# Performance work log

Hardware: AMD Instinct MI355X
Metric: run time of the kernel (lower is better)

The kernel has to match this reference:

```python
import jax, jax.numpy as jnp
import numpy as np

TOP_K = 5


def setup_inputs() -> dict:
    key = jax.random.key(0)
    k1, k2 = jax.random.split(key)
    batch, n_attr, feat_dim = 4096, 64000, 512  # 1000 classes x 64 attrs
    image_features = jax.random.normal(k1, (batch, feat_dim), dtype=jnp.float32)
    # raw (unnormalized) attribute concept features, flattened to (n_attr, feat_dim)
    attr_features = jax.random.normal(k2, (n_attr, feat_dim), dtype=jnp.float32)
    return {"image_features": image_features, "attr_features": attr_features}


def reference(image_features, attr_features):
    # __init__: L2-normalize attribute features along feature dim
    attr_norm = attr_features / jnp.linalg.norm(attr_features, axis=-1, keepdims=True)
    # similarities: (batch, n_attr) dense dot-product matrix
    similarities = image_features @ attr_norm.T
    # top-k along attribute dim
    top_scores, top_indices = jax.lax.top_k(similarities, TOP_K)
    # gather selected attribute vectors: (batch, top_k, feat_dim)
    top_attr_features = attr_norm[top_indices]
    return (top_attr_features, top_scores)
```

## Files before the change

### kernel.cpp

```cpp
#include <hip/hip_runtime.h>
#include <float.h>

#define FEAT 512
#define TOPK 5
#define NSEL 16
#define BM 256
#define BN 256
#define BKT 64
#define NKT (FEAT / BKT)
#define ABYTES (BM * BKT)
#define BUFB (2 * ABYTES)
#define NCB 4

typedef __attribute__((ext_vector_type(4))) int i32x4;

__device__ __forceinline__ void gl_lds16(const void* g, void* lds) {
    __builtin_amdgcn_global_load_lds(
        (const __attribute__((address_space(1))) unsigned int*)g,
        (__attribute__((address_space(3))) unsigned int*)lds, 16, 0, 0);
}

__global__ __launch_bounds__(256) void quant_attr(
    const float* __restrict__ in, signed char* __restrict__ q,
    float* __restrict__ inv) {
    const int w = threadIdx.x >> 6, l = threadIdx.x & 63;
    const int row = blockIdx.x * 4 + w;
    const float4* p = reinterpret_cast<const float4*>(in) + (size_t)row * (FEAT / 4);
    const float4 v0 = p[l * 2], v1 = p[l * 2 + 1];
    float ss = v0.x * v0.x + v0.y * v0.y + v0.z * v0.z + v0.w * v0.w +
               v1.x * v1.x + v1.y * v1.y + v1.z * v1.z + v1.w * v1.w;
#pragma unroll
    for (int m = 1; m < 64; m <<= 1) ss += __shfl_xor(ss, m);
    const float iv = 1.0f / sqrtf(fmaxf(ss, 1e-30f));
    const float qs = iv * 300.0f;
    int qv[8];
    qv[0] = __float2int_rn(v0.x * qs); qv[1] = __float2int_rn(v0.y * qs);
    qv[2] = __float2int_rn(v0.z * qs); qv[3] = __float2int_rn(v0.w * qs);
    qv[4] = __float2int_rn(v1.x * qs); qv[5] = __float2int_rn(v1.y * qs);
    qv[6] = __float2int_rn(v1.z * qs); qv[7] = __float2int_rn(v1.w * qs);
#pragma unroll
    for (int j = 0; j < 8; ++j) qv[j] = min(127, max(-127, qv[j]));
    int2 st;
    st.x = (qv[0] & 255) | ((qv[1] & 255) << 8) | ((qv[2] & 255) << 16) |
           ((unsigned)(qv[3] & 255) << 24);
    st.y = (qv[4] & 255) | ((qv[5] & 255) << 8) | ((qv[6] & 255) << 16) |
           ((unsigned)(qv[7] & 255) << 24);
    *reinterpret_cast<int2*>(q + (size_t)row * FEAT + l * 8) = st;
    if (l == 0) inv[row] = iv;
}

__global__ __launch_bounds__(256) void quant_img(
    const float* __restrict__ in, signed char* __restrict__ q) {
    const int w = threadIdx.x >> 6, l = threadIdx.x & 63;
    const int row = blockIdx.x * 4 + w;
    const float4* p = reinterpret_cast<const float4*>(in) + (size_t)row * (FEAT / 4);
    const float4 v0 = p[l * 2], v1 = p[l * 2 + 1];
    float mx = fmaxf(fmaxf(fmaxf(fabsf(v0.x), fabsf(v0.y)), fmaxf(fabsf(v0.z), fabsf(v0.w))),
                     fmaxf(fmaxf(fabsf(v1.x), fabsf(v1.y)), fmaxf(fabsf(v1.z), fabsf(v1.w))));
#pragma unroll
    for (int m = 1; m < 64; m <<= 1) mx = fmaxf(mx, __shfl_xor(mx, m));
    mx = fmaxf(mx, 1e-20f);
    const float qs = 127.0f / mx;
    const int q0 = __float2int_rn(v0.x * qs), q1 = __float2int_rn(v0.y * qs);
    const int q2 = __float2int_rn(v0.z * qs), q3 = __float2int_rn(v0.w * qs);
    const int q4 = __float2int_rn(v1.x * qs), q5 = __float2int_rn(v1.y * qs);
    const int q6 = __float2int_rn(v1.z * qs), q7 = __float2int_rn(v1.w * qs);
    int2 st;
    st.x = (q0 & 255) | ((q1 & 255) << 8) | ((q2 & 255) << 16) | ((unsigned)(q3 & 255) << 24);
    st.y = (q4 & 255) | ((q5 & 255) << 8) | ((q6 & 255) << 16) | ((unsigned)(q7 & 255) << 24);
    *reinterpret_cast<int2*>(q + (size_t)row * FEAT + l * 8) = st;
}

__global__ __launch_bounds__(512, 2) void coarse_kernel(
    const signed char* __restrict__ attrQ, const signed char* __restrict__ imgQ,
    unsigned* __restrict__ cand, int nablk, int niblk) {
    __shared__ __align__(1024) char lds[2][BUFB];
    const int tid = threadIdx.x;

    const int cpx = gridDim.x >> 3;
    const int wg = ((int)blockIdx.x & 7) * cpx + ((int)blockIdx.x >> 3);
    const int ablock = wg / niblk;
    const int iblock = wg % niblk;

    const int w = tid >> 6, l = tid & 63;
    const int wr = w >> 2, wc = w & 3;
    const int lrow = l & 15, lg = l >> 4;

    const int srow = tid >> 2, sg = tid & 3;
    const int ssw = sg ^ ((srow ^ (srow >> 2)) & 3);
    const signed char* asrc = attrQ + (size_t)(ablock * BM + srow) * FEAT + (ssw << 4);
    const signed char* bsrc = imgQ + (size_t)(iblock * BN + srow) * FEAT + (ssw << 4);

    int a_off[8], b_off[4];
#pragma unroll
    for (int m = 0; m < 8; ++m) {
        const int r = wr * 128 + m * 16 + lrow;
        a_off[m] = r * BKT + ((lg ^ ((r ^ (r >> 2)) & 3)) << 4);
    }
#pragma unroll
    for (int n = 0; n < 4; ++n) {
        const int r = wc * 64 + n * 16 + lrow;
        b_off[n] = ABYTES + r * BKT + ((lg ^ ((r ^ (r >> 2)) & 3)) << 4);
    }

    i32x4 acc[8][4];
#pragma unroll
    for (int m = 0; m < 8; ++m)
#pragma unroll
        for (int n = 0; n < 4; ++n) acc[m][n] = (i32x4){0, 0, 0, 0};

#define STAGE(bufi, kt)                                                      \
    {                                                                        \
        char* d_ = &lds[bufi][tid * 16];                                     \
        gl_lds16(asrc + (kt) * BKT, d_);                                     \
        gl_lds16(asrc + (kt) * BKT + (size_t)128 * FEAT, d_ + 8192);         \
        gl_lds16(bsrc + (kt) * BKT, d_ + 16384);                             \
        gl_lds16(bsrc + (kt) * BKT + (size_t)128 * FEAT, d_ + 24576);        \
    }

    STAGE(0, 0);
#pragma unroll 1
    for (int t = 0; t < NKT; ++t) {
        const int cur = t & 1;
        const char* buf = &lds[cur][0];
        if (t < NKT - 1) STAGE(cur ^ 1, t + 1);
        __builtin_amdgcn_sched_barrier(0);
        if (t < NKT - 1) {
            asm volatile("s_waitcnt vmcnt(4)" ::: "memory");
        } else {
            asm volatile("s_waitcnt vmcnt(0)" ::: "memory");
        }
        __builtin_amdgcn_s_barrier();
        __builtin_amdgcn_sched_barrier(0);

        i32x4 bF[4];
#pragma unroll
        for (int n = 0; n < 4; ++n)
            bF[n] = *reinterpret_cast<const i32x4*>(buf + b_off[n]);

#pragma unroll
        for (int p = 0; p < 4; ++p) {
            const i32x4 aF0 = *reinterpret_cast<const i32x4*>(buf + a_off[2 * p]);
            const i32x4 aF1 = *reinterpret_cast<const i32x4*>(buf + a_off[2 * p + 1]);
            asm volatile("s_waitcnt lgkmcnt(0)" ::: "memory");
            __builtin_amdgcn_sched_barrier(0);
            __builtin_amdgcn_s_setprio(1);
#pragma unroll
            for (int n = 0; n < 4; ++n)
                acc[2 * p][n] = __builtin_amdgcn_mfma_i32_16x16x64_i8(
                    aF0, bF[n], acc[2 * p][n], 0, 0, 0);
#pragma unroll
            for (int n = 0; n < 4; ++n)
                acc[2 * p + 1][n] = __builtin_amdgcn_mfma_i32_16x16x64_i8(
                    aF1, bF[n], acc[2 * p + 1][n], 0, 0, 0);
            __builtin_amdgcn_s_setprio(0);
            __builtin_amdgcn_sched_barrier(0);
        }
        __builtin_amdgcn_s_barrier();
        __builtin_amdgcn_sched_barrier(0);
    }
#undef STAGE

    unsigned m1[4] = {0u, 0u, 0u, 0u}, m2[4] = {0u, 0u, 0u, 0u};
#pragma unroll
    for (int m = 0; m < 8; ++m)
#pragma unroll
        for (int r = 0; r < 4; ++r) {
            const int rowl = wr * 128 + m * 16 + lg * 4 + r;
            const unsigned idxc = 2047u - (unsigned)rowl;
#pragma unroll
            for (int n = 0; n < 4; ++n) {
                const unsigned p =
                    (((unsigned)(acc[m][n][r] + (1 << 23)) << 8) & 0xFFFFF800u) | idxc;
                m2[n] = max(m2[n], min(m1[n], p));
                m1[n] = max(m1[n], p);
            }
        }

    unsigned* scratch = reinterpret_cast<unsigned*>(&lds[0][0]);
#pragma unroll
    for (int n = 0; n < 4; ++n) {
        scratch[(w * 64 + l) * 8 + n * 2] = m1[n];
        scratch[(w * 64 + l) * 8 + n * 2 + 1] = m2[n];
    }
    __syncthreads();

    if (tid < BN) {
        const int wc2 = tid >> 6, cw = tid & 63;
        const int n = cw >> 4, lr = cw & 15;
        unsigned best[NCB] = {0u, 0u, 0u, 0u};
#pragma unroll
        for (int wr2 = 0; wr2 < 2; ++wr2)
#pragma unroll
            for (int lg2 = 0; lg2 < 4; ++lg2)
#pragma unroll
                for (int k = 0; k < 2; ++k) {
                    const unsigned p =
                        scratch[((wr2 * 4 + wc2) * 64 + lg2 * 16 + lr) * 8 + n * 2 + k];
                    if (p > best[NCB - 1]) {
                        best[NCB - 1] = p;
#pragma unroll
                        for (int x = NCB - 1; x > 0; --x)
                            if (best[x] > best[x - 1]) {
                                const unsigned t_ = best[x];
                                best[x] = best[x - 1]; best[x - 1] = t_;
                            }
                    }
                }
        const size_t base = ((size_t)(iblock * BN + tid) * nablk + ablock) * NCB;
#pragma unroll
        for (int j = 0; j < NCB; ++j) cand[base + j] = best[j];
    }
}

__global__ __launch_bounds__(64) void select16_kernel(
    const unsigned* __restrict__ cand, int* __restrict__ sel, int nablk) {
    const int row = blockIdx.x;
    const int l = threadIdx.x;
    const int ncand = nablk * NCB;
    const unsigned* cr = cand + (size_t)row * ncand;
    unsigned p[16]; int c[16];
#pragma unroll
    for (int j = 0; j < 16; ++j) {
        const int slot = l * 16 + j;
        if (slot < ncand) {
            const unsigned v = cr[slot];
            p[j] = v;
            c[j] = (slot / NCB) * BM + (2047 - (int)(v & 0x7FFu));
        } else { p[j] = 0u; c[j] = 0x7fffffff; }
    }
    int* out = sel + (size_t)row * NSEL;
    for (int r = 0; r < NSEL; ++r) {
        unsigned bp = 0u; int bc = 0x7fffffff;
#pragma unroll
        for (int j = 0; j < 16; ++j)
            if (p[j] > bp || (p[j] == bp && c[j] < bc)) { bp = p[j]; bc = c[j]; }
#pragma unroll
        for (int m = 1; m < 64; m <<= 1) {
            const unsigned op = __shfl_xor(bp, m);
            const int oc = __shfl_xor(bc, m);
            if (op > bp || (op == bp && oc < bc)) { bp = op; bc = oc; }
        }
        if (l == 0) out[r] = bc;
#pragma unroll
        for (int j = 0; j < 16; ++j)
            if (p[j] == bp && c[j] == bc) { p[j] = 0u; c[j] = 0x7fffffff; }
    }
}

__global__ __launch_bounds__(256) void rescore_kernel(
    const float* __restrict__ img, const float* __restrict__ attr,
    const float* __restrict__ inv, const int* __restrict__ sel,
    float* __restrict__ out_scores, int* __restrict__ final_i) {
    __shared__ float s_sc[NSEL];
    const int row = blockIdx.x;
    const int w = threadIdx.x >> 6, l = threadIdx.x & 63;
    const float4* ip = reinterpret_cast<const float4*>(img) + (size_t)row * (FEAT / 4);
    const float4 a0 = ip[l * 2], a1 = ip[l * 2 + 1];
#pragma unroll
    for (int q = 0; q < 4; ++q) {
        const int slot = w * 4 + q;
        const int ci = sel[(size_t)row * NSEL + slot];
        const float4* ap = reinterpret_cast<const float4*>(attr) + (size_t)ci * (FEAT / 4);
        const float4 b0 = ap[l * 2], b1 = ap[l * 2 + 1];
        float d = a0.x * b0.x + a0.y * b0.y + a0.z * b0.z + a0.w * b0.w +
                  a1.x * b1.x + a1.y * b1.y + a1.z * b1.z + a1.w * b1.w;
#pragma unroll
        for (int m = 1; m < 64; m <<= 1) d += __shfl_xor(d, m);
        if (l == 0) s_sc[slot] = d * inv[ci];
    }
    __syncthreads();
    if (threadIdx.x == 0) {
        float ts[TOPK]; int ti[TOPK];
#pragma unroll
        for (int j = 0; j < TOPK; ++j) { ts[j] = -FLT_MAX; ti[j] = 0x7fffffff; }
        for (int e = 0; e < NSEL; ++e) {
            const float sv = s_sc[e];
            const int iv = sel[(size_t)row * NSEL + e];
            if (sv > ts[4] || (sv == ts[4] && iv < ti[4])) {
                ts[4] = sv; ti[4] = iv;
#pragma unroll
                for (int x = 4; x > 0; --x)
                    if (ts[x] > ts[x - 1] || (ts[x] == ts[x - 1] && ti[x] < ti[x - 1])) {
                        const float tf = ts[x]; ts[x] = ts[x - 1]; ts[x - 1] = tf;
                        const int td = ti[x]; ti[x] = ti[x - 1]; ti[x - 1] = td;
                    }
            }
        }
#pragma unroll
        for (int j = 0; j < TOPK; ++j) {
            out_scores[(size_t)row * TOPK + j] = ts[j];
            final_i[(size_t)row * TOPK + j] = ti[j];
        }
    }
}

__global__ __launch_bounds__(128) void gather_kernel(
    const float* __restrict__ attr, const float* __restrict__ inv,
    const int* __restrict__ final_i, float* __restrict__ out0) {
    const int pair = blockIdx.x;
    const int fi = final_i[pair];
    const float sc = inv[fi];
    const float4 v =
        reinterpret_cast<const float4*>(attr)[(size_t)fi * (FEAT / 4) + threadIdx.x];
    float4 o;
    o.x = v.x * sc; o.y = v.y * sc; o.z = v.z * sc; o.w = v.w * sc;
    reinterpret_cast<float4*>(out0)[(size_t)pair * (FEAT / 4) + threadIdx.x] = o;
}

extern "C" void kernel_launch(void* const* d_in, const int* in_sizes, int n_in,
                              void* d_out, int out_size, void* d_ws, size_t ws_size,
                              hipStream_t stream) {
    const float* img = (const float*)d_in[0];
    const float* attr = (const float*)d_in[1];
    const int batch = in_sizes[0] / FEAT;
    const int nattr = in_sizes[1] / FEAT;
    const int nablk = nattr / BM;
    const int niblk = batch / BN;

    char* ws = (char*)d_ws;
    signed char* attrQ = (signed char*)ws; ws += (size_t)nattr * FEAT;
    signed char* imgQ = (signed char*)ws;  ws += (size_t)batch * FEAT;
    float* inv = (float*)ws;               ws += (size_t)nattr * 4;
    unsigned* cand = (unsigned*)ws;        ws += (size_t)batch * nablk * NCB * 4;
    int* sel = (int*)ws;                   ws += (size_t)batch * NSEL * 4;
    int* final_i = (int*)ws;               ws += (size_t)batch * TOPK * 4;

    float* out0 = (float*)d_out;
    float* out_scores = out0 + (size_t)batch * TOPK * FEAT;

    quant_attr<<<nattr / 4, 256, 0, stream>>>(attr, attrQ, inv);
    quant_img<<<batch / 4, 256, 0, stream>>>(img, imgQ);
    coarse_kernel<<<nablk * niblk, 512, 0, stream>>>(attrQ, imgQ, cand, nablk, niblk);
    select16_kernel<<<batch, 64, 0, stream>>>(cand, sel, nablk);
    rescore_kernel<<<batch, 256, 0, stream>>>(img, attr, inv, sel, out_scores, final_i);
    gather_kernel<<<batch * TOPK, 128, 0, stream>>>(attr, inv, final_i, out0);
}
```

Before: 278.6 us.

## Triple-buffer coarse GEMM LDS staging and interleave global loads with MFMA phases

Switches the int8 coarse GEMM from double to triple LDS buffering, prefetching two k-tiles ahead. Global-to-LDS loads are spread across the four MFMA sub-phases, with a barrier around each phase, and the k-loop is fully unrolled. This is meant to hide global load latency better. In exchange, LDS per block grows to 96KB, which may reduce the number of resident blocks per CU, and the count of workgroup barriers rises.

```diff
diff --git a/kernel.cpp b/kernel.cpp
--- a/kernel.cpp
+++ b/kernel.cpp
@@ -74,7 +74,7 @@
 __global__ __launch_bounds__(512, 2) void coarse_kernel(
     const signed char* __restrict__ attrQ, const signed char* __restrict__ imgQ,
     unsigned* __restrict__ cand, int nablk, int niblk) {
-    __shared__ __align__(1024) char lds[2][BUFB];
+    __shared__ __align__(1024) char lds[3][BUFB];
     const int tid = threadIdx.x;
 
     const int cpx = gridDim.x >> 3;
@@ -109,39 +109,48 @@
 #pragma unroll
         for (int n = 0; n < 4; ++n) acc[m][n] = (i32x4){0, 0, 0, 0};
 
-#define STAGE(bufi, kt)                                                      \
-    {                                                                        \
-        char* d_ = &lds[bufi][tid * 16];                                     \
-        gl_lds16(asrc + (kt) * BKT, d_);                                     \
-        gl_lds16(asrc + (kt) * BKT + (size_t)128 * FEAT, d_ + 8192);         \
-        gl_lds16(bsrc + (kt) * BKT, d_ + 16384);                             \
-        gl_lds16(bsrc + (kt) * BKT + (size_t)128 * FEAT, d_ + 24576);        \
-    }
-
-    STAGE(0, 0);
-#pragma unroll 1
+#pragma unroll
+    for (int h = 0; h < 4; ++h) {
+        const signed char* s_ = (h < 2 ? asrc : bsrc) + (size_t)(h & 1) * 128 * FEAT;
+        gl_lds16(s_, &lds[0][h * 8192 + tid * 16]);
+    }
+#pragma unroll
+    for (int h = 0; h < 4; ++h) {
+        const signed char* s_ = (h < 2 ? asrc : bsrc) + (size_t)(h & 1) * 128 * FEAT + BKT;
+        gl_lds16(s_, &lds[1][h * 8192 + tid * 16]);
+    }
+    asm volatile("s_waitcnt vmcnt(4)" ::: "memory");
+    __builtin_amdgcn_s_barrier();
+    __builtin_amdgcn_sched_barrier(0);
+
+#pragma unroll
     for (int t = 0; t < NKT; ++t) {
-        const int cur = t & 1;
-        const char* buf = &lds[cur][0];
-        if (t < NKT - 1) STAGE(cur ^ 1, t + 1);
-        __builtin_amdgcn_sched_barrier(0);
-        if (t < NKT - 1) {
-            asm volatile("s_waitcnt vmcnt(4)" ::: "memory");
-        } else {
-            asm volatile("s_waitcnt vmcnt(0)" ::: "memory");
-        }
-        __builtin_amdgcn_s_barrier();
-        __builtin_amdgcn_sched_barrier(0);
-
+        const char* buf = &lds[t % 3][0];
+        char* sdst = &lds[(t + 2) % 3][0];
         i32x4 bF[4];
 #pragma unroll
-        for (int n = 0; n < 4; ++n)
-            bF[n] = *reinterpret_cast<const i32x4*>(buf + b_off[n]);
-
-#pragma unroll
         for (int p = 0; p < 4; ++p) {
+            if (p == 0) {
+#pragma unroll
+                for (int n = 0; n < 4; ++n)
+                    bF[n] = *reinterpret_cast<const i32x4*>(buf + b_off[n]);
+            }
             const i32x4 aF0 = *reinterpret_cast<const i32x4*>(buf + a_off[2 * p]);
             const i32x4 aF1 = *reinterpret_cast<const i32x4*>(buf + a_off[2 * p + 1]);
+            if (t + 2 < NKT) {
+                const signed char* s_ =
+                    (p < 2 ? asrc : bsrc) + (size_t)(p & 1) * 128 * FEAT + (t + 2) * BKT;
+                gl_lds16(s_, sdst + p * 8192 + tid * 16);
+            }
+            if (p == 3) {
+                if (t < NKT - 2) {
+                    asm volatile("s_waitcnt vmcnt(4)" ::: "memory");
+                } else if (t == NKT - 2) {
+                    asm volatile("s_waitcnt vmcnt(0)" ::: "memory");
+                }
+            }
+            __builtin_amdgcn_sched_barrier(0);
+            __builtin_amdgcn_s_barrier();
             asm volatile("s_waitcnt lgkmcnt(0)" ::: "memory");
             __builtin_amdgcn_sched_barrier(0);
             __builtin_amdgcn_s_setprio(1);
@@ -155,11 +164,10 @@
                     aF1, bF[n], acc[2 * p + 1][n], 0, 0, 0);
             __builtin_amdgcn_s_setprio(0);
             __builtin_amdgcn_sched_barrier(0);
-        }
-        __builtin_amdgcn_s_barrier();
-        __builtin_amdgcn_sched_barrier(0);
-    }
-#undef STAGE
+            __builtin_amdgcn_s_barrier();
+            __builtin_amdgcn_sched_barrier(0);
+        }
+    }
 
     unsigned m1[4] = {0u, 0u, 0u, 0u}, m2[4] = {0u, 0u, 0u, 0u};
 #pragma unroll
```

After: 296.7 us. +6.5%, slower.
